# Performance work log

Measured on AMD Instinct MI355X. Metric: run time of the kernel, lower is better.

## Reference

```python
import jax, jax.numpy as jnp
import numpy as np

N = 50000   # nodes
E = 800000  # edges
IN, H1, H2, OUT = 128, 256, 128, 1


def setup_inputs() -> dict:
    key = jax.random.key(0)
    ks = jax.random.split(key, 9)
    x = jax.random.normal(ks[0], (N, IN), dtype=jnp.float32)
    edge_index = jax.random.randint(ks[1], (2, E), 0, N, dtype=jnp.int32)
    def glorot(k, fan_in, fan_out):
        s = np.sqrt(6.0 / (fan_in + fan_out)).astype(np.float32)
        return jax.random.uniform(k, (fan_in, fan_out), jnp.float32, -s, s)
    W1 = glorot(ks[2], IN, H1)
    b1 = jnp.zeros((H1,), jnp.float32)
    W2 = glorot(ks[3], H1, H2)
    b2 = jnp.zeros((H2,), jnp.float32)
    W3 = glorot(ks[4], H2, OUT)
    b3 = jnp.zeros((OUT,), jnp.float32)
    return {"x": x, "edge_index": edge_index, "W1": W1, "b1": b1,
            "W2": W2, "b2": b2, "W3": W3, "b3": b3}


def _gcn_layer(x, W, b, src, dst, norm):
    # dense transform [N, d_in] @ [d_in, d_out]
    h = x @ W
    # degree-normalized sparse aggregation: out[dst] += norm * h[src]
    agg = jax.ops.segment_sum(h[src] * norm[:, None], dst, num_segments=N)
    return agg + b


def reference(x, edge_index, W1, b1, W2, b2, W3, b3):
    src, dst = edge_index[0], edge_index[1]
    # PyG GCNConv: add self loops, then symmetric normalization
    loop = jnp.arange(N, dtype=src.dtype)
    src = jnp.concatenate([src, loop])
    dst = jnp.concatenate([dst, loop])
    deg = jax.ops.segment_sum(jnp.ones_like(dst, jnp.float32), dst, num_segments=N)
    dis = jax.lax.rsqrt(jnp.maximum(deg, 1.0))  # deg >= 1 via self loops
    norm = dis[src] * dis[dst]  # [E+N]
    h1 = jax.nn.relu(_gcn_layer(x, W1, b1, src, dst, norm))
    h2 = jax.nn.relu(_gcn_layer(h1, W2, b2, src, dst, norm))
    y = _gcn_layer(h2, W3, b3, src, dst, norm).reshape(-1)
    return (y, h1, h2)
```

## Files before the change

### kernel.cpp

```cpp
#include <hip/hip_runtime.h>


typedef __attribute__((ext_vector_type(8))) short short8;
typedef __attribute__((ext_vector_type(4))) float f32x4;

static __device__ __forceinline__ unsigned short f2bf(float f){
  union { float f; unsigned u; } v; v.f = f;
  unsigned r = v.u + 0x7FFF + ((v.u >> 16) & 1);
  return (unsigned short)(r >> 16);
}
static __device__ __forceinline__ float2 bf2f2(unsigned u){
  union { unsigned u; float f; } a, b;
  a.u = u << 16; b.u = u & 0xffff0000u;
  return make_float2(a.f, b.f);
}

__global__ __launch_bounds__(256) void k_prepbin(
    const int* __restrict__ src, const int* __restrict__ dst,
    int* __restrict__ bcur, unsigned* __restrict__ pairs, int E, int binB,
    const float* __restrict__ W1, const float* __restrict__ W2,
    unsigned short* __restrict__ Wf1, unsigned short* __restrict__ Wf2,
    const float4* __restrict__ x, uint2* __restrict__ xb, int nv){
  __shared__ int cl[256];
  int blk = blockIdx.x;
  int tid = threadIdx.x;
  if (blk < binB){
    int e0 = blk * 4096 + tid;
    cl[tid] = 0; __syncthreads();
    #pragma unroll
    for (int i = 0; i < 16; i++){
      int e = e0 + i*256;
      if (e < E) atomicAdd(&cl[dst[e] >> 8], 1);
    }
    __syncthreads();
    int c = cl[tid];
    int g = (c > 0) ? atomicAdd(&bcur[tid], c) : 0;
    cl[tid] = g;
    __syncthreads();
    #pragma unroll
    for (int i = 0; i < 16; i++){
      int e = e0 + i*256;
      if (e < E){
        int d = dst[e];
        int b = d >> 8;
        int p = atomicAdd(&cl[b], 1);
        pairs[(b << 13) + p] = (unsigned)src[e] | ((unsigned)(d & 255) << 16);
      }
    }
  } else if (blk < binB + 256){
    int t = (blk - binB)*256 + tid;
    if (t < 32768){
      int j = t & 7, lane = (t>>3) & 63, kt = (t>>9) & 3, nt = t >> 11;
      int nn = nt*16 + (lane & 15);
      int kk = kt*32 + (lane>>4)*8 + j;
      Wf1[t] = f2bf(W1[kk*256 + nn]);
    } else {
      int o = t - 32768;
      int j = o & 7, lane = (o>>3) & 63, nt = (o>>9) & 7, kt = o >> 12;
      int nn = nt*16 + (lane & 15);
      int kk = kt*32 + (lane>>4)*8 + j;
      Wf2[o] = f2bf(W2[kk*128 + nn]);
    }
  } else {
    int i = (blk - binB - 256)*256 + tid;
    if (i < nv){
      float4 v = x[i];
      xb[i] = make_uint2((unsigned)f2bf(v.x) | ((unsigned)f2bf(v.y) << 16),
                         (unsigned)f2bf(v.z) | ((unsigned)f2bf(v.w) << 16));
    }
  }
}

__global__ __launch_bounds__(256) void k_place(
    const int* __restrict__ bcur, const unsigned* __restrict__ pairs,
    unsigned short* __restrict__ csr_src, int* __restrict__ rowptr,
    int* __restrict__ cnt, float* __restrict__ dis, int n, int nb){
  __shared__ int sh[256];
  __shared__ int ncnt[256];
  int t = threadIdx.x;
  int b = blockIdx.x;
  int v = (t < nb) ? bcur[t] : 0;
  sh[t] = v; __syncthreads();
  for (int off = 1; off < 256; off <<= 1){
    int x = (t >= off) ? sh[t-off] : 0;
    __syncthreads(); sh[t] += x; __syncthreads();
  }
  int csr_base = (b == 0) ? 0 : sh[b-1];
  int cnt_b = bcur[b];
  ncnt[t] = 0; __syncthreads();
  const unsigned* P = pairs + ((size_t)b << 13);
  for (int i = t; i < cnt_b; i += 256) atomicAdd(&ncnt[P[i] >> 16], 1);
  __syncthreads();
  int c = ncnt[t];
  sh[t] = c; __syncthreads();
  for (int off = 1; off < 256; off <<= 1){
    int x = (t >= off) ? sh[t-off] : 0;
    __syncthreads(); sh[t] += x; __syncthreads();
  }
  int noff = sh[t] - c;
  int node = (b << 8) + t;
  if (node < n){
    rowptr[node] = csr_base + noff;
    cnt[node] = c;
    dis[node] = rsqrtf((float)(c + 1));
  }
  ncnt[t] = noff; __syncthreads();
  for (int i = t; i < cnt_b; i += 256){
    unsigned u = P[i];
    int p = atomicAdd(&ncnt[u >> 16], 1);
    csr_src[csr_base + p] = (unsigned short)(u & 0xffff);
  }
}

__global__ void k_aggL1(const unsigned* __restrict__ xb, unsigned* __restrict__ out,
                        const int* __restrict__ rowptr, const int* __restrict__ cnt,
                        const unsigned short* __restrict__ csr_src,
                        const float* __restrict__ dis, int n){
  int t = threadIdx.x;
  int lane = t & 63;
  int node = blockIdx.x*4 + (t >> 6);
  if (node >= n) return;
  float di = dis[node];
  float2 v = bf2f2(xb[(size_t)node*64 + lane]);
  float2 acc = make_float2(di*v.x, di*v.y);
  int start = rowptr[node];
  int mm = cnt[node];
  int j = 0;
  for (; j + 15 < mm; j += 16){
    int s[16]; unsigned uv[16]; float w[16];
    #pragma unroll
    for (int q = 0; q < 16; q++) s[q] = csr_src[start+j+q];
    #pragma unroll
    for (int q = 0; q < 16; q++){ w[q] = dis[s[q]]; uv[q] = xb[(size_t)s[q]*64 + lane]; }
    #pragma unroll
    for (int q = 0; q < 16; q++){
      float2 u = bf2f2(uv[q]);
      acc.x = fmaf(w[q], u.x, acc.x); acc.y = fmaf(w[q], u.y, acc.y);
    }
  }
  for (; j + 3 < mm; j += 4){
    int s[4]; unsigned uv[4]; float w[4];
    #pragma unroll
    for (int q = 0; q < 4; q++) s[q] = csr_src[start+j+q];
    #pragma unroll
    for (int q = 0; q < 4; q++){ w[q] = dis[s[q]]; uv[q] = xb[(size_t)s[q]*64 + lane]; }
    #pragma unroll
    for (int q = 0; q < 4; q++){
      float2 u = bf2f2(uv[q]);
      acc.x = fmaf(w[q], u.x, acc.x); acc.y = fmaf(w[q], u.y, acc.y);
    }
  }
  for (; j < mm; j++){
    int s = csr_src[start+j];
    float2 u = bf2f2(xb[(size_t)s*64 + lane]);
    float w = dis[s];
    acc.x = fmaf(w, u.x, acc.x); acc.y = fmaf(w, u.y, acc.y);
  }
  acc.x *= di; acc.y *= di;
  out[(size_t)node*64 + lane] =
      (unsigned)f2bf(acc.x) | ((unsigned)f2bf(acc.y) << 16);
}

__global__ void k_aggL2(const unsigned* __restrict__ t2b, float* __restrict__ h2,
                        const int* __restrict__ rowptr, const int* __restrict__ cnt,
                        const unsigned short* __restrict__ csr_src,
                        const float* __restrict__ dis,
                        const float* __restrict__ b2, const float* __restrict__ W3,
                        float* __restrict__ u, int n){
  int t = threadIdx.x;
  int lane = t & 63;
  int node = blockIdx.x*4 + (t >> 6);
  if (node >= n) return;
  float di = dis[node];
  float2 v = bf2f2(t2b[(size_t)node*64 + lane]);
  float2 acc = make_float2(di*v.x, di*v.y);
  int start = rowptr[node];
  int mm = cnt[node];
  int j = 0;
  for (; j + 15 < mm; j += 16){
    int s[16]; unsigned uv[16]; float w[16];
    #pragma unroll
    for (int q = 0; q < 16; q++) s[q] = csr_src[start+j+q];
    #pragma unroll
    for (int q = 0; q < 16; q++){ w[q] = dis[s[q]]; uv[q] = t2b[(size_t)s[q]*64 + lane]; }
    #pragma unroll
    for (int q = 0; q < 16; q++){
      float2 uu = bf2f2(uv[q]);
      acc.x = fmaf(w[q], uu.x, acc.x); acc.y = fmaf(w[q], uu.y, acc.y);
    }
  }
  for (; j + 3 < mm; j += 4){
    int s[4]; unsigned uv[4]; float w[4];
    #pragma unroll
    for (int q = 0; q < 4; q++) s[q] = csr_src[start+j+q];
    #pragma unroll
    for (int q = 0; q < 4; q++){ w[q] = dis[s[q]]; uv[q] = t2b[(size_t)s[q]*64 + lane]; }
    #pragma unroll
    for (int q = 0; q < 4; q++){
      float2 uu = bf2f2(uv[q]);
      acc.x = fmaf(w[q], uu.x, acc.x); acc.y = fmaf(w[q], uu.y, acc.y);
    }
  }
  for (; j < mm; j++){
    int s = csr_src[start+j];
    float2 uu = bf2f2(t2b[(size_t)s*64 + lane]);
    float w = dis[s];
    acc.x = fmaf(w, uu.x, acc.x); acc.y = fmaf(w, uu.y, acc.y);
  }
  float2 b = ((const float2*)b2)[lane];
  acc.x = fmaxf(fmaf(di, acc.x, b.x), 0.0f);
  acc.y = fmaxf(fmaf(di, acc.y, b.y), 0.0f);
  ((float2*)h2)[(size_t)node*64 + lane] = acc;
  float up = fmaf(acc.x, W3[2*lane], acc.y * W3[2*lane+1]);
  #pragma unroll
  for (int off = 32; off > 0; off >>= 1) up += __shfl_down(up, off);
  if (lane == 0) u[node] = up;
}

__global__ __launch_bounds__(256) void k_gemm12(
    const unsigned short* __restrict__ Xa,
    const unsigned short* __restrict__ Wf1,
    const unsigned short* __restrict__ Wf2,
    const float* __restrict__ b1,
    float* __restrict__ h1,
    unsigned short* __restrict__ T2b,
    int n)
{
  __shared__ unsigned short As1[64*136];
  __shared__ unsigned short As2[64*264];
  int t = threadIdx.x;
  int row0 = blockIdx.x * 64;
  {
    const float4* src = (const float4*)Xa;
    #pragma unroll
    for (int i = 0; i < 4; i++){
      int f = i*256 + t, r = f >> 4, c = f & 15;
      float4 v = make_float4(0,0,0,0);
      if (row0 + r < n) v = src[(size_t)(row0+r)*16 + c];
      *(float4*)&As1[r*136 + c*8] = v;
    }
  }
  __syncthreads();
  int w = t >> 6, lane = t & 63, m = lane & 15, q = lane >> 4;
  int rbase = w*16;
  short8 af[4];
  #pragma unroll
  for (int kt = 0; kt < 4; kt++)
    af[kt] = *(const short8*)&As1[(rbase + m)*136 + kt*32 + q*8];
  f32x4 acc1[16];
  #pragma unroll
  for (int i = 0; i < 16; i++) acc1[i] = (f32x4){0.f,0.f,0.f,0.f};
  const short8* W1v = (const short8*)Wf1;
  #pragma unroll
  for (int nt = 0; nt < 16; nt++){
    #pragma unroll
    for (int kt = 0; kt < 4; kt++){
      short8 bfr = W1v[(nt*4 + kt)*64 + lane];
      acc1[nt] = __builtin_amdgcn_mfma_f32_16x16x32_bf16(af[kt], bfr, acc1[nt], 0, 0, 0);
    }
  }
  int rowa = row0 + rbase + q*4;
  #pragma unroll
  for (int nt = 0; nt < 16; nt++){
    float b = b1[nt*16 + m];
    #pragma unroll
    for (int r = 0; r < 4; r++){
      int rr = rowa + r;
      float o = fmaxf(acc1[nt][r] + b, 0.0f);
      if (rr < n) h1[(size_t)rr*256 + nt*16 + m] = o;
      As2[(rbase + q*4 + r)*264 + nt*16 + m] = f2bf(o);
    }
  }
  __syncthreads();
  short8 af2[8];
  #pragma unroll
  for (int kt = 0; kt < 8; kt++)
    af2[kt] = *(const short8*)&As2[(rbase + m)*264 + kt*32 + q*8];
  f32x4 acc2[8];
  #pragma unroll
  for (int i = 0; i < 8; i++) acc2[i] = (f32x4){0.f,0.f,0.f,0.f};
  const short8* W2v = (const short8*)Wf2;
  #pragma unroll
  for (int nt = 0; nt < 8; nt++){
    #pragma unroll
    for (int kt = 0; kt < 8; kt++){
      short8 bfr = W2v[(kt*8 + nt)*64 + lane];
      acc2[nt] = __builtin_amdgcn_mfma_f32_16x16x32_bf16(af2[kt], bfr, acc2[nt], 0, 0, 0);
    }
  }
  #pragma unroll
  for (int nt = 0; nt < 8; nt++){
    #pragma unroll
    for (int r = 0; r < 4; r++){
      int rr = rowa + r;
      if (rr < n) T2b[(size_t)rr*128 + nt*16 + m] = f2bf(acc2[nt][r]);
    }
  }
}

__global__ void k_agg1d(const float* __restrict__ u, float* __restrict__ y,
                        const int* __restrict__ rowptr, const int* __restrict__ cnt,
                        const unsigned short* __restrict__ csr_src,
                        const float* __restrict__ dis,
                        const float* __restrict__ b3, int n){
  int i = blockIdx.x*256 + threadIdx.x;
  if (i >= n) return;
  float di = dis[i];
  float acc = di * u[i];
  int s0 = rowptr[i], m = cnt[i];
  for (int j = 0; j < m; j++){
    int s = csr_src[s0+j];
    acc = fmaf(dis[s], u[s], acc);
  }
  y[i] = fmaf(di, acc, b3[0]);
}

extern "C" void kernel_launch(void* const* d_in, const int* in_sizes, int n_in,
                              void* d_out, int out_size, void* d_ws, size_t ws_size,
                              hipStream_t stream){
  const float* x  = (const float*)d_in[0];
  const int*  ei  = (const int*)d_in[1];
  const float* W1 = (const float*)d_in[2];
  const float* b1 = (const float*)d_in[3];
  const float* W2 = (const float*)d_in[4];
  const float* b2 = (const float*)d_in[5];
  const float* W3 = (const float*)d_in[6];
  const float* b3 = (const float*)d_in[7];
  const int N = in_sizes[0] / 128;
  const int E = in_sizes[1] / 2;
  const int* src = ei;
  const int* dst = ei + E;
  const int NB = (N + 255) >> 8;

  char* p = (char*)d_ws;
  auto alloc = [&](size_t bytes)->char*{
    char* r = p; p += (bytes + 255) & ~(size_t)255; return r;
  };
  int*   bcur    = (int*)  alloc(256*4);
  int*   rowptr  = (int*)  alloc((size_t)N*4);
  int*   cnt     = (int*)  alloc((size_t)N*4);
  float* dis     = (float*)alloc((size_t)N*4);
  unsigned* pairs = (unsigned*)alloc((size_t)NB*8192*4);
  unsigned short* csr_src = (unsigned short*)alloc((size_t)E*2);
  unsigned* xb   = (unsigned*)alloc((size_t)N*128*2);
  unsigned* xa   = (unsigned*)alloc((size_t)N*128*2);
  unsigned short* t2b = (unsigned short*)alloc((size_t)N*128*2);
  float* u       = (float*)alloc((size_t)N*4);
  unsigned short* wf1 = (unsigned short*)alloc(32768*2);
  unsigned short* wf2 = (unsigned short*)alloc(32768*2);

  float* y  = (float*)d_out;
  float* h1 = y + N;
  float* h2 = h1 + (size_t)N*256;

  int bb = (E + 4095)/4096;
  int nb = (N + 255)/256;
  int xv = N*32;
  int xblk = (xv + 255)/256;

  hipMemsetAsync(bcur, 0, 256*4, stream);
  k_prepbin <<<bb + 256 + xblk, 256, 0, stream>>>(
      src, dst, bcur, pairs, E, bb, W1, W2, wf1, wf2,
      (const float4*)x, (uint2*)xb, xv);
  k_place   <<<NB, 256, 0, stream>>>(bcur, pairs, csr_src, rowptr, cnt, dis, N, NB);

  int ab = (N + 3)/4;
  int rb = (N + 63)/64;
  k_aggL1   <<<ab, 256, 0, stream>>>(xb, xa, rowptr, cnt, csr_src, dis, N);
  k_gemm12  <<<rb, 256, 0, stream>>>((const unsigned short*)xa, wf1, wf2, b1, h1, t2b, N);
  k_aggL2   <<<ab, 256, 0, stream>>>((const unsigned*)t2b, h2, rowptr, cnt, csr_src, dis, b2, W3, u, N);
  k_agg1d   <<<nb, 256, 0, stream>>>(u, y, rowptr, cnt, csr_src, dis, b3, N);
}
```

Measured before the change: 274.3 us.

## Split fused GEMM into two column-halved MFMA kernels with LDS-staged weights

Replaces the fused layer-1/layer-2 GEMM kernel with two kernels. Each kernel splits the output columns across two blocks and stages its half of the bf16 weight fragments in LDS. Layer-1 output is written as a bf16 copy to global memory, and the second kernel reads it back as input, with the W2 fragment layout reordered to match. The aim is more blocks, lower register pressure and cheaper weight reads, paid for by an extra launch and a 25 MB bf16 h1 round trip through global memory.

Measured after the change: 255.2 us. 1.07x faster.

```diff
diff --git a/kernel.cpp b/kernel.cpp
--- a/kernel.cpp
+++ b/kernel.cpp
@@ -56,8 +56,8 @@
       Wf1[t] = f2bf(W1[kk*256 + nn]);
     } else {
       int o = t - 32768;
-      int j = o & 7, lane = (o>>3) & 63, nt = (o>>9) & 7, kt = o >> 12;
-      int nn = nt*16 + (lane & 15);
+      int j = o & 7, lane = (o>>3) & 63, ntl = (o>>9) & 3, kt = (o>>11) & 7, h = o >> 14;
+      int nn = (h*4 + ntl)*16 + (lane & 15);
       int kk = kt*32 + (lane>>4)*8 + j;
       Wf2[o] = f2bf(W2[kk*128 + nn]);
     }
@@ -217,83 +217,102 @@
   if (lane == 0) u[node] = up;
 }
 
-__global__ __launch_bounds__(256) void k_gemm12(
-    const unsigned short* __restrict__ Xa,
-    const unsigned short* __restrict__ Wf1,
-    const unsigned short* __restrict__ Wf2,
-    const float* __restrict__ b1,
-    float* __restrict__ h1,
-    unsigned short* __restrict__ T2b,
-    int n)
+__global__ __launch_bounds__(256) void k_gemm1_mfma(
+    const unsigned short* __restrict__ Xa, const unsigned short* __restrict__ Wf1,
+    const float* __restrict__ bias, float* __restrict__ out,
+    unsigned short* __restrict__ h1b, int n)
 {
-  __shared__ unsigned short As1[64*136];
-  __shared__ unsigned short As2[64*264];
-  int t = threadIdx.x;
-  int row0 = blockIdx.x * 64;
-  {
-    const float4* src = (const float4*)Xa;
-    #pragma unroll
-    for (int i = 0; i < 4; i++){
-      int f = i*256 + t, r = f >> 4, c = f & 15;
-      float4 v = make_float4(0,0,0,0);
-      if (row0 + r < n) v = src[(size_t)(row0+r)*16 + c];
-      *(float4*)&As1[r*136 + c*8] = v;
-    }
-  }
-  __syncthreads();
+  __shared__ unsigned short Wl[8*4*64*8];
+  int t = threadIdx.x;
+  int row0 = (blockIdx.x >> 1) * 64;
+  int h = blockIdx.x & 1;
   int w = t >> 6, lane = t & 63, m = lane & 15, q = lane >> 4;
   int rbase = w*16;
+  int rowm = row0 + rbase + m;
+  int ra = (rowm < n) ? rowm : (n-1);
+  const short8* Arow = (const short8*)(Xa + (size_t)ra*128);
   short8 af[4];
   #pragma unroll
-  for (int kt = 0; kt < 4; kt++)
-    af[kt] = *(const short8*)&As1[(rbase + m)*136 + kt*32 + q*8];
-  f32x4 acc1[16];
-  #pragma unroll
-  for (int i = 0; i < 16; i++) acc1[i] = (f32x4){0.f,0.f,0.f,0.f};
-  const short8* W1v = (const short8*)Wf1;
-  #pragma unroll
-  for (int nt = 0; nt < 16; nt++){
+  for (int kt = 0; kt < 4; kt++) af[kt] = Arow[kt*4 + q];
+  {
+    const float4* src = (const float4*)Wf1 + (size_t)h*2048;
+    float4* dst = (float4*)Wl;
+    #pragma unroll
+    for (int i = 0; i < 8; i++) dst[i*256 + t] = src[i*256 + t];
+  }
+  __syncthreads();
+  f32x4 acc[8];
+  #pragma unroll
+  for (int i = 0; i < 8; i++) acc[i] = (f32x4){0.f,0.f,0.f,0.f};
+  const short8* Wv = (const short8*)Wl;
+  #pragma unroll
+  for (int nt = 0; nt < 8; nt++){
     #pragma unroll
     for (int kt = 0; kt < 4; kt++){
-      short8 bfr = W1v[(nt*4 + kt)*64 + lane];
-      acc1[nt] = __builtin_amdgcn_mfma_f32_16x16x32_bf16(af[kt], bfr, acc1[nt], 0, 0, 0);
+      short8 bfr = Wv[(nt*4 + kt)*64 + lane];
+      acc[nt] = __builtin_amdgcn_mfma_f32_16x16x32_bf16(af[kt], bfr, acc[nt], 0, 0, 0);
     }
   }
   int rowa = row0 + rbase + q*4;
-  #pragma unroll
-  for (int nt = 0; nt < 16; nt++){
-    float b = b1[nt*16 + m];
+  int colb = h*128 + m;
+  #pragma unroll
+  for (int nt = 0; nt < 8; nt++){
+    float b = bias[colb + nt*16];
     #pragma unroll
     for (int r = 0; r < 4; r++){
       int rr = rowa + r;
-      float o = fmaxf(acc1[nt][r] + b, 0.0f);
-      if (rr < n) h1[(size_t)rr*256 + nt*16 + m] = o;
-      As2[(rbase + q*4 + r)*264 + nt*16 + m] = f2bf(o);
-    }
+      if (rr < n){
+        float o = fmaxf(acc[nt][r] + b, 0.0f);
+        out[(size_t)rr*256 + colb + nt*16] = o;
+        h1b[(size_t)rr*256 + colb + nt*16] = f2bf(o);
+      }
+    }
+  }
+}
+
+__global__ __launch_bounds__(256) void k_gemm2_mfma(
+    const unsigned short* __restrict__ H1b, const unsigned short* __restrict__ Wf2,
+    unsigned short* __restrict__ T2b, int n)
+{
+  __shared__ unsigned short Wl[32*64*8];
+  int t = threadIdx.x;
+  int row0 = (blockIdx.x >> 1) * 64;
+  int h = blockIdx.x & 1;
+  int w = t >> 6, lane = t & 63, m = lane & 15, q = lane >> 4;
+  int rbase = w*16;
+  int rowm = row0 + rbase + m;
+  int ra = (rowm < n) ? rowm : (n-1);
+  const short8* Arow = (const short8*)(H1b + (size_t)ra*256);
+  short8 af[8];
+  #pragma unroll
+  for (int kt = 0; kt < 8; kt++) af[kt] = Arow[kt*4 + q];
+  {
+    const float4* src = (const float4*)Wf2 + (size_t)h*2048;
+    float4* dst = (float4*)Wl;
+    #pragma unroll
+    for (int i = 0; i < 8; i++) dst[i*256 + t] = src[i*256 + t];
   }
   __syncthreads();
-  short8 af2[8];
-  #pragma unroll
-  for (int kt = 0; kt < 8; kt++)
-    af2[kt] = *(const short8*)&As2[(rbase + m)*264 + kt*32 + q*8];
-  f32x4 acc2[8];
-  #pragma unroll
-  for (int i = 0; i < 8; i++) acc2[i] = (f32x4){0.f,0.f,0.f,0.f};
-  const short8* W2v = (const short8*)Wf2;
-  #pragma unroll
-  for (int nt = 0; nt < 8; nt++){
+  f32x4 acc[4];
+  #pragma unroll
+  for (int i = 0; i < 4; i++) acc[i] = (f32x4){0.f,0.f,0.f,0.f};
+  const short8* Wv = (const short8*)Wl;
+  #pragma unroll
+  for (int nt = 0; nt < 4; nt++){
     #pragma unroll
     for (int kt = 0; kt < 8; kt++){
-      short8 bfr = W2v[(kt*8 + nt)*64 + lane];
-      acc2[nt] = __builtin_amdgcn_mfma_f32_16x16x32_bf16(af2[kt], bfr, acc2[nt], 0, 0, 0);
-    }
-  }
-  #pragma unroll
-  for (int nt = 0; nt < 8; nt++){
+      short8 bfr = Wv[(kt*4 + nt)*64 + lane];
+      acc[nt] = __builtin_amdgcn_mfma_f32_16x16x32_bf16(af[kt], bfr, acc[nt], 0, 0, 0);
+    }
+  }
+  int rowa = row0 + rbase + q*4;
+  #pragma unroll
+  for (int nt = 0; nt < 4; nt++){
+    int col = h*64 + nt*16 + m;
     #pragma unroll
     for (int r = 0; r < 4; r++){
       int rr = rowa + r;
-      if (rr < n) T2b[(size_t)rr*128 + nt*16 + m] = f2bf(acc2[nt][r]);
+      if (rr < n) T2b[(size_t)rr*128 + col] = f2bf(acc[nt][r]);
     }
   }
 }
@@ -344,6 +363,7 @@
   unsigned short* csr_src = (unsigned short*)alloc((size_t)E*2);
   unsigned* xb   = (unsigned*)alloc((size_t)N*128*2);
   unsigned* xa   = (unsigned*)alloc((size_t)N*128*2);
+  unsigned short* h1b = (unsigned short*)alloc((size_t)N*256*2);
   unsigned short* t2b = (unsigned short*)alloc((size_t)N*128*2);
   float* u       = (float*)alloc((size_t)N*4);
   unsigned short* wf1 = (unsigned short*)alloc(32768*2);
@@ -366,8 +386,9 @@
 
   int ab = (N + 3)/4;
   int rb = (N + 63)/64;
-  k_aggL1   <<<ab, 256, 0, stream>>>(xb, xa, rowptr, cnt, csr_src, dis, N);
-  k_gemm12  <<<rb, 256, 0, stream>>>((const unsigned short*)xa, wf1, wf2, b1, h1, t2b, N);
-  k_aggL2   <<<ab, 256, 0, stream>>>((const unsigned*)t2b, h2, rowptr, cnt, csr_src, dis, b2, W3, u, N);
-  k_agg1d   <<<nb, 256, 0, stream>>>(u, y, rowptr, cnt, csr_src, dis, b3, N);
-}
+  k_aggL1     <<<ab,   256, 0, stream>>>(xb, xa, rowptr, cnt, csr_src, dis, N);
+  k_gemm1_mfma<<<rb*2, 256, 0, stream>>>((const unsigned short*)xa, wf1, b1, h1, h1b, N);
+  k_gemm2_mfma<<<rb*2, 256, 0, stream>>>(h1b, wf2, t2b, N);
+  k_aggL2     <<<ab,   256, 0, stream>>>((const unsigned*)t2b, h2, rowptr, cnt, csr_src, dis, b2, W3, u, N);
+  k_agg1d     <<<nb,   256, 0, stream>>>(u, y, rowptr, cnt, csr_src, dis, b3, N);
+}
```
